# Performance work log

Measured on AMD Instinct MI355X. Metric: run time of the kernel, lower is better.

## Reference

```python
import jax, jax.numpy as jnp
import numpy as np

CODEBOOK_BITS = 8      # log2(256)
NUM_Q = 2              # NUM_QUANTIZERS
INV_TEMP = 100.0       # LFQ default inv_temperature
DIVERSITY_GAMMA = 1.0
ENTROPY_WEIGHT = 0.1   # LFQ default entropy_loss_weight
COMMIT_WEIGHT = 1.0


def conv2d(x, w, b, pad):
    out = jax.lax.conv_general_dilated(
        x, w, (1, 1), [(pad, pad), (pad, pad)],
        dimension_numbers=('NCHW', 'OIHW', 'NCHW'))
    return out + b[None, :, None, None]


def maxpool2(x):
    return jax.lax.reduce_window(x, -jnp.inf, jax.lax.max,
                                 (1, 1, 2, 2), (1, 1, 2, 2), 'VALID')


def groupnorm(x, groups=4, eps=1e-5):
    B, C, H, W = x.shape
    xg = x.reshape(B, groups, C // groups, H, W)
    mu = xg.mean(axis=(2, 3, 4), keepdims=True)
    var = xg.var(axis=(2, 3, 4), keepdims=True)
    return ((xg - mu) * jax.lax.rsqrt(var + eps)).reshape(B, C, H, W)


def upsample2(x):  # nearest, scale 2
    return jnp.repeat(jnp.repeat(x, 2, axis=2), 2, axis=3)


def lfq_codebook():
    # all 2^8 sign patterns, code j has bit i = ((j>>i)&1)*2-1
    j = jnp.arange(2 ** CODEBOOK_BITS)
    bits = ((j[:, None] >> jnp.arange(CODEBOOK_BITS)[None, :]) & 1).astype(jnp.float32)
    return bits * 2.0 - 1.0  # [256, 8]


def lfq_residual(z):
    # z: (B, D, H, W) with D = CODEBOOK_BITS
    codebook = lfq_codebook()
    t = jnp.transpose(z, (0, 2, 3, 1))  # (B,H,W,D) tokens
    residual = t
    quantized_out = jnp.zeros_like(t)
    pow2 = (2 ** jnp.arange(CODEBOOK_BITS)).astype(jnp.int32)
    indices = []
    aux = jnp.zeros((), t.dtype)
    for _ in range(NUM_Q):
        q_hard = jnp.where(residual > 0, 1.0, -1.0).astype(t.dtype)
        # straight-through binarization
        q = residual + jax.lax.stop_gradient(q_hard - residual)
        idx = jnp.sum((q_hard > 0).astype(jnp.int32) * pow2, axis=-1)  # (B,H,W)
        logits = (2.0 * INV_TEMP) * jnp.einsum('bhwd,cd->bhwc', residual, codebook)
        logp = jax.nn.log_softmax(logits, axis=-1)
        probs = jnp.exp(logp)
        per_sample_entropy = -jnp.mean(jnp.sum(probs * logp, axis=-1))
        avg_prob = jnp.mean(probs.reshape(-1, probs.shape[-1]), axis=0)
        codebook_entropy = -jnp.sum(avg_prob * jnp.log(avg_prob + 1e-10))
        entropy_aux = per_sample_entropy - DIVERSITY_GAMMA * codebook_entropy
        commit = jnp.mean((residual - jax.lax.stop_gradient(q_hard)) ** 2)
        aux = aux + ENTROPY_WEIGHT * entropy_aux + COMMIT_WEIGHT * commit
        quantized_out = quantized_out + q
        residual = residual - jax.lax.stop_gradient(q)
        indices.append(idx)
    q_out = jnp.transpose(quantized_out, (0, 3, 1, 2))  # (B,D,H,W)
    return q_out, jnp.stack(indices, axis=-1), aux


def setup_inputs() -> dict:
    key = jax.random.key(0)
    ks = jax.random.split(key, 13)
    s = 0.05
    return {
        'x': jax.random.normal(ks[0], (32, 1, 256, 256), jnp.float32),
        'w1': jax.random.normal(ks[1], (16, 1, 3, 3), jnp.float32) * s,
        'b1': jax.random.normal(ks[2], (16,), jnp.float32) * s,
        'w2': jax.random.normal(ks[3], (32, 16, 3, 3), jnp.float32) * s,
        'b2': jax.random.normal(ks[4], (32,), jnp.float32) * s,
        'w3': jax.random.normal(ks[5], (8, 32, 1, 1), jnp.float32) * s,
        'b3': jax.random.normal(ks[6], (8,), jnp.float32) * s,
        'd1': jax.random.normal(ks[7], (32, 8, 3, 3), jnp.float32) * s,
        'db1': jax.random.normal(ks[8], (32,), jnp.float32) * s,
        'd2': jax.random.normal(ks[9], (16, 32, 3, 3), jnp.float32) * s,
        'db2': jax.random.normal(ks[10], (16,), jnp.float32) * s,
        'd3': jax.random.normal(ks[11], (1, 16, 3, 3), jnp.float32) * s,
        'db3': jax.random.normal(ks[12], (1,), jnp.float32) * s,
    }


def reference(x, w1, b1, w2, b2, w3, b3, d1, db1, d2, db2, d3, db3):
    # encode
    h = jax.nn.gelu(maxpool2(conv2d(x, w1, b1, pad=1)), approximate=False)
    h = groupnorm(maxpool2(conv2d(h, w2, b2, pad=1)))
    h = conv2d(h, w3, b3, pad=0)  # (B,8,64,64)
    # residual LFQ
    q, indices, aux = lfq_residual(h)
    # decode
    y = upsample2(conv2d(q, d1, db1, pad=1))
    y = upsample2(jax.nn.gelu(conv2d(y, d2, db2, pad=1), approximate=False))
    y = conv2d(y, d3, db3, pad=1)
    return jnp.clip(y, -1.0, 1.0), indices, aux
```

## Files before the change

kernel.cpp:

```cpp
#include <hip/hip_runtime.h>
#include <hip/hip_bf16.h>
#include <math.h>

#define DEV __device__ __forceinline__

DEV float gelu_exact(float x){ return 0.5f*x*(1.0f + erff(x*0.70710678118654752f)); }

__global__ __launch_bounds__(512) void k_prep(const float* __restrict__ w2,
    const float* __restrict__ d2, float* __restrict__ w2t, float* __restrict__ wp4d2)
{
  const int t=threadIdx.x;
  for(int i=t;i<4608;i+=512){
    int oc=i/144, rem=i-oc*144, ic=rem/9, k=rem-ic*9;
    w2t[(ic*32+oc)*9+k]=w2[i];
  }
  for(int i=t;i<2048;i+=512){
    int par=i>>9, ic=(i>>4)&31, oc=i&15;
    int py=par>>1, px=par&1;
    const float* wg = d2 + ((size_t)oc*32+ic)*9;
    float a00=0.f,a01=0.f,a10=0.f,a11=0.f;
    #pragma unroll
    for(int ky=0;ky<3;ky++){
      int sy = py ? (ky>>1) : ((ky>0)?1:0);
      #pragma unroll
      for(int kx=0;kx<3;kx++){
        int sx = px ? (kx>>1) : ((kx>0)?1:0);
        float wv=wg[ky*3+kx];
        if(sy==0){ if(sx==0)a00+=wv; else a01+=wv; }
        else     { if(sx==0)a10+=wv; else a11+=wv; }
      }
    }
    float* dst=wp4d2+(size_t)i*4;
    dst[0]=a00; dst[1]=a01; dst[2]=a10; dst[3]=a11;
  }
}

__global__ __launch_bounds__(256) void k_conv1(const float* __restrict__ x,
    const float* __restrict__ w1, const float* __restrict__ b1,
    float* __restrict__ h1)
{
  __shared__ float sE[34*19], sO[34*19];
  const int b = blockIdx.z;
  const int r0 = blockIdx.x*32, c0 = blockIdx.y*32;
  const float* xp = x + (size_t)b*65536;
  for(int i=threadIdx.x;i<34*34;i+=256){
    int r=i/34, c=i-r*34;
    int gr=r0+r-1, gc=c0+c-1;
    float v=0.f;
    if(gr>=0 && gr<256 && gc>=0 && gc<256) v = xp[gr*256+gc];
    if(c&1) sO[r*19+(c>>1)]=v; else sE[r*19+(c>>1)]=v;
  }
  __syncthreads();
  const int tx=threadIdx.x&15, ty=threadIdx.x>>4;
  const int base = 2*ty*19 + tx;
  float in[4][4];
  #pragma unroll
  for(int r=0;r<4;r++){
    in[r][0]=sE[base+r*19]; in[r][1]=sO[base+r*19];
    in[r][2]=sE[base+r*19+1]; in[r][3]=sO[base+r*19+1];
  }
  const int py = blockIdx.x*16+ty, px = blockIdx.y*16+tx;
  float* op = h1 + ((size_t)b*16)*16384 + py*128 + px;
  #pragma unroll
  for(int ch=0;ch<16;ch++){
    float m=-1e30f;
    #pragma unroll
    for(int pr=0;pr<2;pr++)
      #pragma unroll
      for(int pc=0;pc<2;pc++){
        float a=0.f;
        #pragma unroll
        for(int ky=0;ky<3;ky++)
          #pragma unroll
          for(int kx=0;kx<3;kx++)
            a = fmaf(in[pr+ky][pc+kx], w1[ch*9+ky*3+kx], a);
        m = fmaxf(m,a);
      }
    op[(size_t)ch*16384] = gelu_exact(m + b1[ch]);
  }
}

__global__ __launch_bounds__(256) void k_conv2(const float* __restrict__ h1,
    const float* __restrict__ w2t, const float* __restrict__ b2,
    float* __restrict__ h2, double* __restrict__ pb)
{
  __shared__ __align__(16) float t2[16*360];
  const int b=blockIdx.z;
  const int r0=blockIdx.x*16, c0=blockIdx.y*16;
  const float* hp = h1 + (size_t)b*16*16384;
  for(int i=threadIdx.x;i<2592;i+=256){
    int ic=i/162, rem=i-ic*162, lr=rem/9, jp=rem-lr*9;
    int gr=r0+lr-1, gc=c0+2*jp-1;
    float v0=0.f, v1=0.f;
    if(gr>=0&&gr<128){
      const float* row=hp+(size_t)ic*16384+(size_t)gr*128;
      if(gc>=0&&gc<128) v0=row[gc];
      if(gc+1<128)      v1=row[gc+1];
    }
    *(float2*)&t2[ic*360+lr*20+2*jp]=make_float2(v0,v1);
  }
  __syncthreads();
  const int pos=threadIdx.x&63;
  const int ocg=__builtin_amdgcn_readfirstlane((int)(threadIdx.x>>6));
  const int oc0=ocg*8;
  const int pyl=pos>>3, pxl=pos&7;
  const int base0 = 2*pyl*20 + 2*pxl;
  float acc[8][4];
  #pragma unroll
  for(int o=0;o<8;o++)
    #pragma unroll
    for(int j=0;j<4;j++) acc[o][j]=0.f;
  #pragma unroll 4
  for(int ic=0;ic<16;ic++){
    float in[4][4];
    #pragma unroll
    for(int r=0;r<4;r++){
      float2 a=*(const float2*)&t2[ic*360 + base0 + r*20];
      float2 c=*(const float2*)&t2[ic*360 + base0 + r*20 + 2];
      in[r][0]=a.x; in[r][1]=a.y; in[r][2]=c.x; in[r][3]=c.y;
    }
    const float* wp = w2t + (ic*32+oc0)*9;
    #pragma unroll
    for(int o=0;o<8;o++){
      #pragma unroll
      for(int pr=0;pr<2;pr++)
        #pragma unroll
        for(int pc=0;pc<2;pc++){
          float s=acc[o][pr*2+pc];
          #pragma unroll
          for(int ky=0;ky<3;ky++)
            #pragma unroll
            for(int kx=0;kx<3;kx++)
              s=fmaf(in[pr+ky][pc+kx], wp[o*9+ky*3+kx], s);
          acc[o][pr*2+pc]=s;
        }
    }
  }
  const int py=blockIdx.x*8+pyl, px=blockIdx.y*8+pxl;
  double s=0.0, s2=0.0;
  #pragma unroll
  for(int o=0;o<8;o++){
    const int oc=oc0+o;
    float m=fmaxf(fmaxf(acc[o][0],acc[o][1]),fmaxf(acc[o][2],acc[o][3]));
    float hv=m+b2[oc];
    h2[(((size_t)b*32+oc)*64+py)*64+px]=hv;
    s += (double)hv; s2 += (double)hv*(double)hv;
  }
  #pragma unroll
  for(int off=32;off;off>>=1){
    s  += __shfl_xor(s,  off, 64);
    s2 += __shfl_xor(s2, off, 64);
  }
  if(pos==0){
    const int bidx = blockIdx.x*8 + blockIdx.y;
    double* p = pb + (((size_t)b*4+ocg)*64 + bidx)*2;
    p[0]=s; p[1]=s2;
  }
}

__global__ __launch_bounds__(64) void k_stats2(const double* __restrict__ pb,
                                               float* __restrict__ stats)
{
  const int bg=blockIdx.x, t=threadIdx.x;
  double s = pb[((size_t)bg*64+t)*2], s2 = pb[((size_t)bg*64+t)*2+1];
  #pragma unroll
  for(int off=32;off;off>>=1){
    s  += __shfl_xor(s,  off, 64);
    s2 += __shfl_xor(s2, off, 64);
  }
  if(t==0){
    double mu=s/32768.0;
    double var=s2/32768.0 - mu*mu;
    stats[bg]=(float)mu;
    stats[128+bg]=(float)(1.0/sqrt(var+1e-5));
  }
}

__global__ __launch_bounds__(256) void k_lfq(const float* __restrict__ h2,
    const float* __restrict__ stats, const float* __restrict__ w3, const float* __restrict__ b3,
    float* __restrict__ qout, float* __restrict__ idxout,
    float* __restrict__ avgp, float* __restrict__ ec)
{
  __shared__ __align__(16) float tabL[16*258];
  __shared__ __align__(16) float tabH[16*258];
  const int blk=blockIdx.x;
  const int b=blk>>4;
  const int t=threadIdx.x;
  const int h=(blk&15)*4 + (t>>6);
  const int w=t&63;
  float mu[4], rs[4];
  #pragma unroll
  for(int g=0;g<4;g++){ mu[g]=stats[b*4+g]; rs[g]=stats[128+b*4+g]; }
  const float* hp = h2 + (size_t)b*131072 + h*64 + w;
  float z[8];
  #pragma unroll
  for(int d=0;d<8;d++) z[d]=b3[d];
  #pragma unroll
  for(int c=0;c<32;c++){
    float xn=(hp[(size_t)c*4096]-mu[c>>3])*rs[c>>3];
    #pragma unroll
    for(int d=0;d<8;d++) z[d]=fmaf(xn, w3[d*32+c], z[d]);
  }
  float r[8], qsum[8];
  #pragma unroll
  for(int d=0;d<8;d++){ r[d]=z[d]; qsum[d]=0.f; }
  float entk[2], comk[2];
  #pragma unroll
  for(int k=0;k<2;k++){
    int idx=0; float ent=0.f, com=0.f;
    float pb0[8], pb1[8];
    #pragma unroll
    for(int d=0;d<8;d++){
      float rv=r[d];
      bool pos = rv>0.f;
      float sgn = pos?1.f:-1.f;
      idx |= (pos?1:0)<<d;
      float dd=rv-sgn; com=fmaf(dd,dd,com);
      float a=400.f*fabsf(rv);
      float e=__expf(-a);
      float p=1.f/(1.f+e);
      ent += a - p*a - __logf(p);
      float pm=p, pq=1.f-p;
      pb1[d]=pos?pm:pq;
      pb0[d]=pos?pq:pm;
      qsum[d]+=sgn;
      r[d]=rv-sgn;
    }
    float lo[16], hi[16];
    lo[0]=pb0[0]; lo[1]=pb1[0];
    lo[2]=lo[0]*pb1[1]; lo[3]=lo[1]*pb1[1]; lo[0]*=pb0[1]; lo[1]*=pb0[1];
    lo[4]=lo[0]*pb1[2]; lo[5]=lo[1]*pb1[2]; lo[6]=lo[2]*pb1[2]; lo[7]=lo[3]*pb1[2];
    lo[0]*=pb0[2]; lo[1]*=pb0[2]; lo[2]*=pb0[2]; lo[3]*=pb0[2];
    lo[8]=lo[0]*pb1[3]; lo[9]=lo[1]*pb1[3]; lo[10]=lo[2]*pb1[3]; lo[11]=lo[3]*pb1[3];
    lo[12]=lo[4]*pb1[3]; lo[13]=lo[5]*pb1[3]; lo[14]=lo[6]*pb1[3]; lo[15]=lo[7]*pb1[3];
    lo[0]*=pb0[3]; lo[1]*=pb0[3]; lo[2]*=pb0[3]; lo[3]*=pb0[3];
    lo[4]*=pb0[3]; lo[5]*=pb0[3]; lo[6]*=pb0[3]; lo[7]*=pb0[3];
    hi[0]=pb0[4]; hi[1]=pb1[4];
    hi[2]=hi[0]*pb1[5]; hi[3]=hi[1]*pb1[5]; hi[0]*=pb0[5]; hi[1]*=pb0[5];
    hi[4]=hi[0]*pb1[6]; hi[5]=hi[1]*pb1[6]; hi[6]=hi[2]*pb1[6]; hi[7]=hi[3]*pb1[6];
    hi[0]*=pb0[6]; hi[1]*=pb0[6]; hi[2]*=pb0[6]; hi[3]*=pb0[6];
    hi[8]=hi[0]*pb1[7]; hi[9]=hi[1]*pb1[7]; hi[10]=hi[2]*pb1[7]; hi[11]=hi[3]*pb1[7];
    hi[12]=hi[4]*pb1[7]; hi[13]=hi[5]*pb1[7]; hi[14]=hi[6]*pb1[7]; hi[15]=hi[7]*pb1[7];
    hi[0]*=pb0[7]; hi[1]*=pb0[7]; hi[2]*=pb0[7]; hi[3]*=pb0[7];
    hi[4]*=pb0[7]; hi[5]*=pb0[7]; hi[6]*=pb0[7]; hi[7]*=pb0[7];
    #pragma unroll
    for(int m=0;m<16;m++){ tabL[m*258+t]=lo[m]; tabH[m*258+t]=hi[m]; }
    __syncthreads();
    float accp=0.f, accq=0.f;
    const int jl=t&15, jh=t>>4;
    const float* Lp=&tabL[jl*258];
    const float* Hp=&tabH[jh*258];
    #pragma unroll 8
    for(int q=0;q<128;q++){
      float2 L=*(const float2*)&Lp[2*q];
      float2 H=*(const float2*)&Hp[2*q];
      accp=fmaf(L.x,H.x,accp); accq=fmaf(L.y,H.y,accq);
    }
    avgp[((size_t)k*512+blk)*256+t]=accp+accq;
    __syncthreads();
    entk[k]=ent; comk[k]=com;
    idxout[((size_t)(b*64+h)*64+w)*2+k]=(float)idx;
  }
  #pragma unroll
  for(int d=0;d<8;d++)
    qout[(((size_t)b*8+d)*64+h)*64+w]=qsum[d];
  tabL[t]=entk[0]; tabL[256+t]=entk[1]; tabL[512+t]=comk[0]; tabL[768+t]=comk[1];
  __syncthreads();
  for(int st=128;st>0;st>>=1){
    if(t<st){ tabL[t]+=tabL[t+st]; tabL[256+t]+=tabL[256+t+st];
              tabL[512+t]+=tabL[512+t+st]; tabL[768+t]+=tabL[768+t+st]; }
    __syncthreads();
  }
  if(t==0){ ec[blk*4+0]=tabL[0]; ec[blk*4+1]=tabL[256]; ec[blk*4+2]=tabL[512]; ec[blk*4+3]=tabL[768]; }
}

__global__ __launch_bounds__(256) void k_red(const float* __restrict__ avgp,
    float* __restrict__ avgs)
{
  const int k=blockIdx.x>>4, c0=(blockIdx.x&15)*16;
  const int col=threadIdx.x&15, rg=threadIdx.x>>4;
  float s=0.f;
  for(int j=0;j<32;j++){
    int blk=rg+16*j;
    s+=avgp[((size_t)k*512+blk)*256+c0+col];
  }
  __shared__ float red[256];
  red[threadIdx.x]=s; __syncthreads();
  for(int st=128;st>=16;st>>=1){
    if(threadIdx.x<st) red[threadIdx.x]+=red[threadIdx.x+st];
    __syncthreads();
  }
  if(threadIdx.x<16) avgs[k*256+c0+threadIdx.x]=red[threadIdx.x];
}

__global__ __launch_bounds__(256) void k_final(const float* __restrict__ avgs,
    const float* __restrict__ ec, float* __restrict__ auxout)
{
  __shared__ double red[256];
  const int t=threadIdx.x;
  double cb=0.0;
  #pragma unroll
  for(int k=0;k<2;k++){
    double ap=(double)avgs[k*256+t]*(1.0/131072.0);
    cb += -(ap*log(ap+1e-10));
  }
  red[t]=cb; __syncthreads();
  for(int st=128;st>0;st>>=1){ if(t<st) red[t]+=red[t+st]; __syncthreads(); }
  double CB=red[0]; __syncthreads();
  double e=0.0,c=0.0;
  for(int blk=t;blk<512;blk+=256){
    e += (double)ec[blk*4+0]+(double)ec[blk*4+1];
    c += (double)ec[blk*4+2]+(double)ec[blk*4+3];
  }
  red[t]=e; __syncthreads();
  for(int st=128;st>0;st>>=1){ if(t<st) red[t]+=red[t+st]; __syncthreads(); }
  double E=red[0]; __syncthreads();
  red[t]=c; __syncthreads();
  for(int st=128;st>0;st>>=1){ if(t<st) red[t]+=red[t+st]; __syncthreads(); }
  if(t==0){
    double C=red[0];
    double aux = 0.1*(E*(1.0/131072.0) - CB) + C*(1.0/1048576.0);
    auxout[0]=(float)aux;
  }
}

__global__ __launch_bounds__(256) void k_dec1(const float* __restrict__ q,
    const float* __restrict__ d1, const float* __restrict__ db1, float* __restrict__ out1)
{
  __shared__ float tile[8*342];
  const int b=blockIdx.z, r0=blockIdx.y*16, c0=blockIdx.x*16;
  const float* qp = q + (size_t)b*8*4096;
  for(int i=threadIdx.x;i<8*324;i+=256){
    int ic=i/324, rem=i-ic*324, r=rem/18, c=rem-r*18;
    int gr=r0+r-1, gc=c0+c-1;
    float v=0.f;
    if(gr>=0&&gr<64&&gc>=0&&gc<64) v=qp[ic*4096+gr*64+gc];
    tile[ic*342+r*19+c]=v;
  }
  __syncthreads();
  const int tx=threadIdx.x&15, ty=threadIdx.x>>4;
  float acc[32];
  #pragma unroll
  for(int o=0;o<32;o++) acc[o]=db1[o];
  #pragma unroll 2
  for(int ic=0;ic<8;ic++){
    float v[9];
    #pragma unroll
    for(int ky=0;ky<3;ky++)
      #pragma unroll
      for(int kx=0;kx<3;kx++)
        v[ky*3+kx]=tile[ic*342+(ty+ky)*19+tx+kx];
    #pragma unroll
    for(int o=0;o<32;o++){
      const float* wp=&d1[(o*8+ic)*9];
      float s=acc[o];
      #pragma unroll
      for(int kk=0;kk<9;kk++) s=fmaf(v[kk],wp[kk],s);
      acc[o]=s;
    }
  }
  float* op = out1 + (size_t)b*32*4096 + (r0+ty)*64 + (c0+tx);
  #pragma unroll
  for(int o=0;o<32;o++) op[(size_t)o*4096]=acc[o];
}

__global__ __launch_bounds__(256) void k_dec2(const float* __restrict__ out1,
    const float* __restrict__ wp4d2, const float* __restrict__ db2, float* __restrict__ out2)
{
  __shared__ float tile[32*342];
  const int b=blockIdx.z, y0=blockIdx.y*32, x0=blockIdx.x*32;
  const int sy0=(y0>>1)-1, sx0=(x0>>1)-1;
  const float* sp = out1 + (size_t)b*32*4096;
  for(int i=threadIdx.x;i<32*324;i+=256){
    int ic=i/324, rem=i-ic*324, r=rem/18, c=rem-r*18;
    int gr=sy0+r, gc=sx0+c;
    float v=0.f;
    if(gr>=0&&gr<64&&gc>=0&&gc<64) v=sp[ic*4096+gr*64+gc];
    tile[ic*342+r*19+c]=v;
  }
  __syncthreads();
  const int par=__builtin_amdgcn_readfirstlane((int)(threadIdx.x>>6));
  const int py=par>>1, px=par&1;
  const int l=threadIdx.x&63, r0l=l>>4, cl=l&15;
  const int bxl=cl+px;
  float acc[16][4];
  #pragma unroll
  for(int o=0;o<16;o++){
    float bv=db2[o];
    #pragma unroll
    for(int a=0;a<4;a++) acc[o][a]=bv;
  }
  #pragma unroll 2
  for(int ic=0;ic<32;ic++){
    const float* wq = wp4d2 + (size_t)((par*32+ic)*16)*4;
    float s00[4],s01[4],s10[4],s11[4];
    #pragma unroll
    for(int a=0;a<4;a++){
      const int byl=r0l+4*a+py;
      const float* tp=&tile[ic*342 + byl*19 + bxl];
      s00[a]=tp[0]; s01[a]=tp[1]; s10[a]=tp[19]; s11[a]=tp[20];
    }
    #pragma unroll
    for(int o=0;o<16;o++){
      const float wx=wq[o*4], wy=wq[o*4+1], wz=wq[o*4+2], ww=wq[o*4+3];
      #pragma unroll
      for(int a=0;a<4;a++)
        acc[o][a]=fmaf(s00[a],wx,fmaf(s01[a],wy,fmaf(s10[a],wz,fmaf(s11[a],ww,acc[o][a]))));
    }
  }
  #pragma unroll
  for(int o=0;o<16;o++){
    float* op = out2 + ((size_t)b*16+o)*16384;
    #pragma unroll
    for(int a=0;a<4;a++){
      const int yy=2*(r0l+4*a)+py, xx=2*cl+px;
      op[(size_t)(y0+yy)*128 + (x0+xx)] = gelu_exact(acc[o][a]);
    }
  }
}

__global__ __launch_bounds__(256) void k_dec3(const float* __restrict__ out2,
    const float* __restrict__ d3, const float* __restrict__ db3, float* __restrict__ y)
{
  __shared__ float tile[16*342];
  __shared__ float4 wp4[64];
  const int b=blockIdx.z, y0=blockIdx.x*32, x0=blockIdx.y*32;
  const int sy0=(y0>>1)-1, sx0=(x0>>1)-1;
  const float* sp = out2 + (size_t)b*16*16384;
  for(int i=threadIdx.x;i<16*324;i+=256){
    int ic=i/324, rem=i-ic*324, r=rem/18, c=rem-r*18;
    int gr=sy0+r, gc=sx0+c;
    float v=0.f;
    if(gr>=0&&gr<128&&gc>=0&&gc<128) v=sp[ic*16384+gr*128+gc];
    tile[ic*342+r*19+c]=v;
  }
  if(threadIdx.x<64){
    int par=threadIdx.x>>4, ic=threadIdx.x&15;
    int py=par>>1, px=par&1;
    const float* wg = d3 + ic*9;
    float a00=0.f,a01=0.f,a10=0.f,a11=0.f;
    #pragma unroll
    for(int ky=0;ky<3;ky++){
      int sy = py ? (ky>>1) : ((ky>0)?1:0);
      #pragma unroll
      for(int kx=0;kx<3;kx++){
        int sx = px ? (kx>>1) : ((kx>0)?1:0);
        float wv=wg[ky*3+kx];
        if(sy==0){ if(sx==0)a00+=wv; else a01+=wv; }
        else     { if(sx==0)a10+=wv; else a11+=wv; }
      }
    }
    wp4[threadIdx.x]=make_float4(a00,a01,a10,a11);
  }
  __syncthreads();
  const float bias=db3[0];
  const int par=__builtin_amdgcn_readfirstlane((int)(threadIdx.x>>6));
  const int py=par>>1, px=par&1;
  const int l=threadIdx.x&63, r0l=l>>4, cl=l&15;
  const int bxl=cl+px;
  float acc[4];
  #pragma unroll
  for(int a=0;a<4;a++) acc[a]=bias;
  #pragma unroll 2
  for(int ic=0;ic<16;ic++){
    const float4 wv=wp4[par*16+ic];
    #pragma unroll
    for(int a=0;a<4;a++){
      const int byl=r0l+4*a+py;
      const float* tp=&tile[ic*342 + byl*19 + bxl];
      acc[a]=fmaf(tp[0],wv.x,fmaf(tp[1],wv.y,fmaf(tp[19],wv.z,fmaf(tp[20],wv.w,acc[a]))));
    }
  }
  #pragma unroll
  for(int a=0;a<4;a++){
    const int yy=2*(r0l+4*a)+py, xx=2*cl+px;
    float v=fminf(fmaxf(acc[a],-1.0f),1.0f);
    y[(size_t)b*65536 + (size_t)(y0+yy)*256 + (x0+xx)] = v;
  }
}

extern "C" void kernel_launch(void* const* d_in, const int* in_sizes, int n_in,
                              void* d_out, int out_size, void* d_ws, size_t ws_size,
                              hipStream_t stream)
{
  const float* x  =(const float*)d_in[0];
  const float* w1 =(const float*)d_in[1];
  const float* b1 =(const float*)d_in[2];
  const float* w2 =(const float*)d_in[3];
  const float* b2 =(const float*)d_in[4];
  const float* w3 =(const float*)d_in[5];
  const float* b3 =(const float*)d_in[6];
  const float* d1 =(const float*)d_in[7];
  const float* db1=(const float*)d_in[8];
  const float* d2 =(const float*)d_in[9];
  const float* db2=(const float*)d_in[10];
  const float* d3 =(const float*)d_in[11];
  const float* db3=(const float*)d_in[12];
  float* out=(float*)d_out;
  float* ws =(float*)d_ws;
  float* h1   = ws;
  float* h2   = ws + 8388608;
  float* qb   = ws + 12582912;
  float* st   = ws + 13631488;
  float* avgp = ws + 13631744;
  float* ec   = ws + 13893888;
  float* w2t  = avgp;
  float* wp4d2= ws + 13895936;
  float* avgs = ws + 13904128;
  double* pb  = (double*)qb;
  float* out1 = h2;
  float* out2 = h1;

  k_prep  <<<dim3(1),512,0,stream>>>(w2,d2,w2t,wp4d2);
  k_conv1 <<<dim3(8,8,32),256,0,stream>>>(x,w1,b1,h1);
  k_conv2 <<<dim3(8,8,32),256,0,stream>>>(h1,w2t,b2,h2,pb);
  k_stats2<<<dim3(128),64,0,stream>>>(pb,st);
  k_lfq   <<<dim3(512),256,0,stream>>>(h2,st,w3,b3,qb,out+2097152,avgp,ec);
  k_red   <<<dim3(32),256,0,stream>>>(avgp,avgs);
  k_final <<<dim3(1),256,0,stream>>>(avgs,ec,out+2359296);
  k_dec1  <<<dim3(4,4,32),256,0,stream>>>(qb,d1,db1,out1);
  k_dec2  <<<dim3(4,4,32),256,0,stream>>>(out1,wp4d2,db2,out2);
  k_dec3  <<<dim3(8,8,32),256,0,stream>>>(out2,d3,db3,out);
}
```

Baseline: 231.3 us.

## Shrink decoder tiles, split conv2 input staging, and parallelize weight prep

k_dec1 and k_dec2 move to 8x8 source tiles with 4x more blocks. Each thread now computes fewer outputs (8 channels in dec1, one position per parity in dec2), which cuts register pressure and LDS size so more waves can be resident. k_conv2 stages its 16 input channels in two halves of 8, halving shared memory at the cost of an extra barrier pair and no overlap of load with compute. k_prep is spread across 8 blocks instead of one. The trade-off is more halo reloading and less reuse of each staged value and weight per thread.

```diff
diff --git a/kernel.cpp b/kernel.cpp
--- a/kernel.cpp
+++ b/kernel.cpp
@@ -6,15 +6,15 @@
 
 DEV float gelu_exact(float x){ return 0.5f*x*(1.0f + erff(x*0.70710678118654752f)); }
 
-__global__ __launch_bounds__(512) void k_prep(const float* __restrict__ w2,
+__global__ __launch_bounds__(256) void k_prep(const float* __restrict__ w2,
     const float* __restrict__ d2, float* __restrict__ w2t, float* __restrict__ wp4d2)
 {
-  const int t=threadIdx.x;
-  for(int i=t;i<4608;i+=512){
+  const int gid = blockIdx.x*256 + threadIdx.x;
+  for(int i=gid;i<4608;i+=2048){
     int oc=i/144, rem=i-oc*144, ic=rem/9, k=rem-ic*9;
     w2t[(ic*32+oc)*9+k]=w2[i];
   }
-  for(int i=t;i<2048;i+=512){
+  for(int i=gid;i<2048;i+=2048){
     int par=i>>9, ic=(i>>4)&31, oc=i&15;
     int py=par>>1, px=par&1;
     const float* wg = d2 + ((size_t)oc*32+ic)*9;
@@ -84,22 +84,10 @@
     const float* __restrict__ w2t, const float* __restrict__ b2,
     float* __restrict__ h2, double* __restrict__ pb)
 {
-  __shared__ __align__(16) float t2[16*360];
+  __shared__ __align__(16) float t2[8*360];
   const int b=blockIdx.z;
   const int r0=blockIdx.x*16, c0=blockIdx.y*16;
   const float* hp = h1 + (size_t)b*16*16384;
-  for(int i=threadIdx.x;i<2592;i+=256){
-    int ic=i/162, rem=i-ic*162, lr=rem/9, jp=rem-lr*9;
-    int gr=r0+lr-1, gc=c0+2*jp-1;
-    float v0=0.f, v1=0.f;
-    if(gr>=0&&gr<128){
-      const float* row=hp+(size_t)ic*16384+(size_t)gr*128;
-      if(gc>=0&&gc<128) v0=row[gc];
-      if(gc+1<128)      v1=row[gc+1];
-    }
-    *(float2*)&t2[ic*360+lr*20+2*jp]=make_float2(v0,v1);
-  }
-  __syncthreads();
   const int pos=threadIdx.x&63;
   const int ocg=__builtin_amdgcn_readfirstlane((int)(threadIdx.x>>6));
   const int oc0=ocg*8;
@@ -110,31 +98,47 @@
   for(int o=0;o<8;o++)
     #pragma unroll
     for(int j=0;j<4;j++) acc[o][j]=0.f;
-  #pragma unroll 4
-  for(int ic=0;ic<16;ic++){
-    float in[4][4];
-    #pragma unroll
-    for(int r=0;r<4;r++){
-      float2 a=*(const float2*)&t2[ic*360 + base0 + r*20];
-      float2 c=*(const float2*)&t2[ic*360 + base0 + r*20 + 2];
-      in[r][0]=a.x; in[r][1]=a.y; in[r][2]=c.x; in[r][3]=c.y;
-    }
-    const float* wp = w2t + (ic*32+oc0)*9;
-    #pragma unroll
-    for(int o=0;o<8;o++){
-      #pragma unroll
-      for(int pr=0;pr<2;pr++)
+
+  for(int half=0;half<2;half++){
+    for(int i=threadIdx.x;i<1296;i+=256){
+      int ic=i/162, rem=i-ic*162, lr=rem/9, jp=rem-lr*9;
+      int gr=r0+lr-1, gc=c0+2*jp-1;
+      float v0=0.f, v1=0.f;
+      if(gr>=0&&gr<128){
+        const float* row=hp+(size_t)(half*8+ic)*16384+(size_t)gr*128;
+        if(gc>=0&&gc<128) v0=row[gc];
+        if(gc+1<128)      v1=row[gc+1];
+      }
+      *(float2*)&t2[ic*360+lr*20+2*jp]=make_float2(v0,v1);
+    }
+    __syncthreads();
+    #pragma unroll 4
+    for(int ic=0;ic<8;ic++){
+      float in[4][4];
+      #pragma unroll
+      for(int r=0;r<4;r++){
+        float2 a=*(const float2*)&t2[ic*360 + base0 + r*20];
+        float2 c=*(const float2*)&t2[ic*360 + base0 + r*20 + 2];
+        in[r][0]=a.x; in[r][1]=a.y; in[r][2]=c.x; in[r][3]=c.y;
+      }
+      const float* wp = w2t + ((half*8+ic)*32+oc0)*9;
+      #pragma unroll
+      for(int o=0;o<8;o++){
         #pragma unroll
-        for(int pc=0;pc<2;pc++){
-          float s=acc[o][pr*2+pc];
+        for(int pr=0;pr<2;pr++)
           #pragma unroll
-          for(int ky=0;ky<3;ky++)
+          for(int pc=0;pc<2;pc++){
+            float s=acc[o][pr*2+pc];
             #pragma unroll
-            for(int kx=0;kx<3;kx++)
-              s=fmaf(in[pr+ky][pc+kx], wp[o*9+ky*3+kx], s);
-          acc[o][pr*2+pc]=s;
-        }
-    }
+            for(int ky=0;ky<3;ky++)
+              #pragma unroll
+              for(int kx=0;kx<3;kx++)
+                s=fmaf(in[pr+ky][pc+kx], wp[o*9+ky*3+kx], s);
+            acc[o][pr*2+pc]=s;
+          }
+      }
+    }
+    __syncthreads();
   }
   const int py=blockIdx.x*8+pyl, px=blockIdx.y*8+pxl;
   double s=0.0, s2=0.0;
@@ -327,21 +331,23 @@
 __global__ __launch_bounds__(256) void k_dec1(const float* __restrict__ q,
     const float* __restrict__ d1, const float* __restrict__ db1, float* __restrict__ out1)
 {
-  __shared__ float tile[8*342];
-  const int b=blockIdx.z, r0=blockIdx.y*16, c0=blockIdx.x*16;
+  __shared__ float tile[8*110];
+  const int b=blockIdx.z, r0=blockIdx.x*8, c0=blockIdx.y*8;
   const float* qp = q + (size_t)b*8*4096;
-  for(int i=threadIdx.x;i<8*324;i+=256){
-    int ic=i/324, rem=i-ic*324, r=rem/18, c=rem-r*18;
+  for(int i=threadIdx.x;i<800;i+=256){
+    int ic=i/100, rem=i-ic*100, r=rem/10, c=rem-r*10;
     int gr=r0+r-1, gc=c0+c-1;
     float v=0.f;
     if(gr>=0&&gr<64&&gc>=0&&gc<64) v=qp[ic*4096+gr*64+gc];
-    tile[ic*342+r*19+c]=v;
+    tile[ic*110+r*11+c]=v;
   }
   __syncthreads();
-  const int tx=threadIdx.x&15, ty=threadIdx.x>>4;
-  float acc[32];
-  #pragma unroll
-  for(int o=0;o<32;o++) acc[o]=db1[o];
+  const int ocg=__builtin_amdgcn_readfirstlane((int)(threadIdx.x>>6));
+  const int oc0=ocg*8;
+  const int l=threadIdx.x&63, ry=l>>3, cx=l&7;
+  float acc[8];
+  #pragma unroll
+  for(int o=0;o<8;o++) acc[o]=db1[oc0+o];
   #pragma unroll 2
   for(int ic=0;ic<8;ic++){
     float v[9];
@@ -349,74 +355,56 @@
     for(int ky=0;ky<3;ky++)
       #pragma unroll
       for(int kx=0;kx<3;kx++)
-        v[ky*3+kx]=tile[ic*342+(ty+ky)*19+tx+kx];
-    #pragma unroll
-    for(int o=0;o<32;o++){
-      const float* wp=&d1[(o*8+ic)*9];
+        v[ky*3+kx]=tile[ic*110+(ry+ky)*11+cx+kx];
+    #pragma unroll
+    for(int o=0;o<8;o++){
+      const float* wp=&d1[((oc0+o)*8+ic)*9];
       float s=acc[o];
       #pragma unroll
       for(int kk=0;kk<9;kk++) s=fmaf(v[kk],wp[kk],s);
       acc[o]=s;
     }
   }
-  float* op = out1 + (size_t)b*32*4096 + (r0+ty)*64 + (c0+tx);
-  #pragma unroll
-  for(int o=0;o<32;o++) op[(size_t)o*4096]=acc[o];
+  #pragma unroll
+  for(int o=0;o<8;o++)
+    out1[(((size_t)b*32+oc0+o)*64 + r0+ry)*64 + c0+cx]=acc[o];
 }
 
 __global__ __launch_bounds__(256) void k_dec2(const float* __restrict__ out1,
     const float* __restrict__ wp4d2, const float* __restrict__ db2, float* __restrict__ out2)
 {
-  __shared__ float tile[32*342];
-  const int b=blockIdx.z, y0=blockIdx.y*32, x0=blockIdx.x*32;
+  __shared__ float tile[32*110];
+  const int b=blockIdx.z, y0=blockIdx.x*16, x0=blockIdx.y*16;
   const int sy0=(y0>>1)-1, sx0=(x0>>1)-1;
   const float* sp = out1 + (size_t)b*32*4096;
-  for(int i=threadIdx.x;i<32*324;i+=256){
-    int ic=i/324, rem=i-ic*324, r=rem/18, c=rem-r*18;
+  for(int i=threadIdx.x;i<3200;i+=256){
+    int ic=i/100, rem=i-ic*100, r=rem/10, c=rem-r*10;
     int gr=sy0+r, gc=sx0+c;
     float v=0.f;
     if(gr>=0&&gr<64&&gc>=0&&gc<64) v=sp[ic*4096+gr*64+gc];
-    tile[ic*342+r*19+c]=v;
+    tile[ic*110+r*11+c]=v;
   }
   __syncthreads();
   const int par=__builtin_amdgcn_readfirstlane((int)(threadIdx.x>>6));
   const int py=par>>1, px=par&1;
-  const int l=threadIdx.x&63, r0l=l>>4, cl=l&15;
-  const int bxl=cl+px;
-  float acc[16][4];
-  #pragma unroll
-  for(int o=0;o<16;o++){
-    float bv=db2[o];
-    #pragma unroll
-    for(int a=0;a<4;a++) acc[o][a]=bv;
-  }
+  const int l=threadIdx.x&63, ry=l>>3, cx=l&7;
+  const int byl=ry+py, bxl=cx+px;
+  float acc[16];
+  #pragma unroll
+  for(int o=0;o<16;o++) acc[o]=db2[o];
   #pragma unroll 2
   for(int ic=0;ic<32;ic++){
+    const float* tp=&tile[ic*110 + byl*11 + bxl];
+    const float s00=tp[0], s01=tp[1], s10=tp[11], s11=tp[12];
     const float* wq = wp4d2 + (size_t)((par*32+ic)*16)*4;
-    float s00[4],s01[4],s10[4],s11[4];
-    #pragma unroll
-    for(int a=0;a<4;a++){
-      const int byl=r0l+4*a+py;
-      const float* tp=&tile[ic*342 + byl*19 + bxl];
-      s00[a]=tp[0]; s01[a]=tp[1]; s10[a]=tp[19]; s11[a]=tp[20];
-    }
-    #pragma unroll
-    for(int o=0;o<16;o++){
-      const float wx=wq[o*4], wy=wq[o*4+1], wz=wq[o*4+2], ww=wq[o*4+3];
-      #pragma unroll
-      for(int a=0;a<4;a++)
-        acc[o][a]=fmaf(s00[a],wx,fmaf(s01[a],wy,fmaf(s10[a],wz,fmaf(s11[a],ww,acc[o][a]))));
-    }
-  }
-  #pragma unroll
-  for(int o=0;o<16;o++){
-    float* op = out2 + ((size_t)b*16+o)*16384;
-    #pragma unroll
-    for(int a=0;a<4;a++){
-      const int yy=2*(r0l+4*a)+py, xx=2*cl+px;
-      op[(size_t)(y0+yy)*128 + (x0+xx)] = gelu_exact(acc[o][a]);
-    }
-  }
+    #pragma unroll
+    for(int o=0;o<16;o++)
+      acc[o]=fmaf(s00,wq[o*4],fmaf(s01,wq[o*4+1],fmaf(s10,wq[o*4+2],fmaf(s11,wq[o*4+3],acc[o]))));
+  }
+  const int Y=y0+2*ry+py, X=x0+2*cx+px;
+  #pragma unroll
+  for(int o=0;o<16;o++)
+    out2[((size_t)b*16+o)*16384 + (size_t)Y*128 + X] = gelu_exact(acc[o]);
 }
 
 __global__ __launch_bounds__(256) void k_dec3(const float* __restrict__ out2,
@@ -511,14 +499,14 @@
   float* out1 = h2;
   float* out2 = h1;
 
-  k_prep  <<<dim3(1),512,0,stream>>>(w2,d2,w2t,wp4d2);
+  k_prep  <<<dim3(8),256,0,stream>>>(w2,d2,w2t,wp4d2);
   k_conv1 <<<dim3(8,8,32),256,0,stream>>>(x,w1,b1,h1);
   k_conv2 <<<dim3(8,8,32),256,0,stream>>>(h1,w2t,b2,h2,pb);
   k_stats2<<<dim3(128),64,0,stream>>>(pb,st);
   k_lfq   <<<dim3(512),256,0,stream>>>(h2,st,w3,b3,qb,out+2097152,avgp,ec);
   k_red   <<<dim3(32),256,0,stream>>>(avgp,avgs);
   k_final <<<dim3(1),256,0,stream>>>(avgs,ec,out+2359296);
-  k_dec1  <<<dim3(4,4,32),256,0,stream>>>(qb,d1,db1,out1);
-  k_dec2  <<<dim3(4,4,32),256,0,stream>>>(out1,wp4d2,db2,out2);
+  k_dec1  <<<dim3(8,8,32),256,0,stream>>>(qb,d1,db1,out1);
+  k_dec2  <<<dim3(8,8,32),256,0,stream>>>(out1,wp4d2,db2,out2);
   k_dec3  <<<dim3(8,8,32),256,0,stream>>>(out2,d3,db3,out);
 }
```

Result: faster. 202.3 us (-12.5%).
